# Performance work log

Hardware: AMD Instinct MI355X
Metric: run time of the kernel (lower is better)

The kernel has to match this reference:

```python
import jax, jax.numpy as jnp
import numpy as np

D_TEXT, D_AUDIO, D_HID = 1024, 768, 1024
EPS = 1e-5


def layer_norm(x, gamma, beta):
    mu = jnp.mean(x, axis=-1, keepdims=True)
    var = jnp.mean(jnp.square(x - mu), axis=-1, keepdims=True)
    return (x - mu) * jax.lax.rsqrt(var + EPS) * gamma + beta


def setup_inputs() -> dict:
    key = jax.random.key(0)
    ks = jax.random.split(key, 8)
    B, L, S = 16, 1024, 2048
    # xavier_uniform bound = sqrt(6/(fan_in+fan_out))
    def xavier(k, shape):
        bound = np.sqrt(6.0 / (shape[0] + shape[1]))
        return jax.random.uniform(k, shape, jnp.float32, -bound, bound)
    return {
        "H_l": jax.random.normal(ks[0], (B, L, D_TEXT), jnp.float32),
        "H_a": jax.random.normal(ks[1], (B, S, D_AUDIO), jnp.float32),
        "W_text": xavier(ks[2], (D_TEXT, D_HID)),
        "b_text": jnp.zeros((D_HID,), jnp.float32),
        "W_audio": xavier(ks[3], (D_AUDIO, D_HID)),
        "b_audio": jnp.zeros((D_HID,), jnp.float32),
        "W_out": xavier(ks[4], (D_HID, D_HID)),
        "b_out": jnp.zeros((D_HID,), jnp.float32),
        "g1": jnp.ones((D_HID,), jnp.float32),
        "beta1": jnp.zeros((D_HID,), jnp.float32),
        "g2": jnp.ones((D_HID,), jnp.float32),
        "beta2": jnp.zeros((D_HID,), jnp.float32),
        "g_out": jnp.ones((D_HID,), jnp.float32),
        "beta_out": jnp.zeros((D_HID,), jnp.float32),
    }


def reference(H_l, H_a, W_text, b_text, W_audio, b_audio, W_out, b_out,
              g1, beta1, g2, beta2, g_out, beta_out):
    # projections
    text_p = jnp.einsum('bld,dh->blh', H_l, W_text) + b_text    # [B,L,H]
    audio_p = jnp.einsum('bsd,dh->bsh', H_a, W_audio) + b_audio  # [B,S,H]
    Q = layer_norm(text_p, g1, beta1)
    K = layer_norm(audio_p, g2, beta2)
    V = audio_p
    scale = 1.0 / np.sqrt(D_HID).astype(np.float32)
    scores = jnp.einsum('blh,bsh->bls', Q, K) * scale            # [B,L,S]
    alpha = jax.nn.softmax(scores, axis=-1)
    # dropout is identity in eval mode
    H_hyper = jnp.einsum('bls,bsh->blh', alpha, V)               # [B,L,H]
    H_hyper = jnp.einsum('blh,hk->blk', H_hyper, W_out) + b_out
    return layer_norm(H_hyper + H_l, g_out, beta_out)
```

## Files before the change

### kernel.cpp

```cpp
#include <hip/hip_runtime.h>
#include <cstdio>

typedef unsigned short u16;
typedef __bf16 bf16x8 __attribute__((ext_vector_type(8)));
typedef float f32x4 __attribute__((ext_vector_type(4)));
typedef unsigned short us4 __attribute__((ext_vector_type(4)));
typedef unsigned short us8 __attribute__((ext_vector_type(8)));

__device__ __forceinline__ u16 f2bf(float f) {
    union { float f; unsigned u; } x; x.f = f;
    unsigned u = x.u + 0x7fffu + ((x.u >> 16) & 1u);
    return (u16)(u >> 16);
}
__device__ __forceinline__ float bf2f(u16 u) {
    union { unsigned u; float f; } x; x.u = ((unsigned)u) << 16;
    return x.f;
}


#define LDFRAG(base, row, koff) \
  (*(const bf16x8*)((const char*)(base) + (size_t)(row) * 128 + \
                    ((koff) ^ (((row) & 7) << 4))))

#define BAR() do { \
  asm volatile("" ::: "memory"); \
  __builtin_amdgcn_s_barrier(); \
  asm volatile("" ::: "memory"); \
} while (0)

#define LGKM0() asm volatile("s_waitcnt lgkmcnt(0)" ::: "memory")

#define MFMA16(AF, BF, MO, NO) do { \
  __builtin_amdgcn_s_setprio(1); \
  _Pragma("unroll") for (int j = 0; j < 4; ++j) \
    _Pragma("unroll") for (int i = 0; i < 2; ++i) \
      _Pragma("unroll") for (int ks = 0; ks < 2; ++ks) \
        acc[(MO) + j][(NO) + i] = __builtin_amdgcn_mfma_f32_16x16x32_bf16( \
            AF[j][ks], BF[i][ks], acc[(MO) + j][(NO) + i], 0, 0, 0); \
  __builtin_amdgcn_s_setprio(0); \
} while (0)

template<int TAG, bool HAS_BIAS, bool HAS_RESID, bool OUT_BF16, bool EMIT_VT>
__global__ __launch_bounds__(512, 2)
void gemm_nt(const u16* __restrict__ A, const u16* __restrict__ Bm,
             void* __restrict__ Cm, const float* __restrict__ bias,
             const float* __restrict__ resid, u16* __restrict__ vt,
             int K, int lda, int ldb, int ldc,
             long sA, long sB, long sC, float scale)
{
    __shared__ __align__(16) u16 lA[4 * 128 * 64];
    __shared__ __align__(16) u16 lB[4 * 128 * 64];

    const int tid = threadIdx.x;

    const int gx = gridDim.x, gy = gridDim.y;
    int flat = ((int)blockIdx.z * gy + blockIdx.y) * gx + blockIdx.x;
    const int nwg = gx * gy * (int)gridDim.z;
    const int q = nwg >> 3;
    flat = (flat & 7) * q + (flat >> 3);
    const int bx = flat % gx;
    const int t2 = flat / gx;
    const int by = t2 % gy;
    const long bz = t2 / gy;

    A  += bz * sA;
    Bm += bz * sB;
    const long cbase = bz * sC;
    const int m0 = by * 256;
    const int n0 = bx * 256;

    const int lane = tid & 63;
    const int w  = tid >> 6;
    const int wr = w >> 2, wc = w & 3;
    const int fr = lane & 15;
    const int kg = lane >> 4;

    auto stage_half = [&](int kt, int op, int h) {
        const u16* src = op ? Bm : A;
        const int  ld  = op ? ldb : lda;
        const int  bs  = op ? n0 : m0;
        u16* lds = (op ? lB : lA) + (size_t)(((2 * kt + h) & 3)) * 8192;
#pragma unroll
        for (int i2 = 0; i2 < 2; ++i2) {
            const int c  = i2 * 512 + tid;
            const int r  = c >> 3;
            const int kb = ((c & 7) * 16) ^ ((r & 7) << 4);
            const u16* g = src + (size_t)(bs + h * 128 + r) * ld + kt * 64 + (kb >> 1);
            __builtin_amdgcn_global_load_lds(
                (const __attribute__((address_space(1))) void*)g,
                (__attribute__((address_space(3))) void*)(lds + (size_t)c * 8), 16, 0, 0);
        }
    };
    auto stage_tile = [&](int kt) {
        stage_half(kt, 0, 0); stage_half(kt, 0, 1);
        stage_half(kt, 1, 0); stage_half(kt, 1, 1);
    };

    f32x4 acc[8][4] = {};

    const int nt = K >> 6;
    stage_tile(0);
    stage_tile(1);

    const int bRowBase = (wc & 1) * 64;

    for (int T = 0; T < nt; ++T) {
        if (T == nt - 1) asm volatile("s_waitcnt vmcnt(0)" ::: "memory");
        else             asm volatile("s_waitcnt vmcnt(8)" ::: "memory");
        BAR();

        const u16* pA = lA + (size_t)(((2 * T + wr) & 3)) * 8192;
        const u16* pB = lB + (size_t)(((2 * T + (wc >> 1)) & 3)) * 8192;
        const bool pre = (T + 2 < nt);

        bf16x8 af0[4][2], af1[4][2], bfr0[2][2], bfr1[2][2];

#pragma unroll
        for (int j = 0; j < 4; ++j)
#pragma unroll
            for (int ks = 0; ks < 2; ++ks)
                af0[j][ks] = LDFRAG(pA, j * 16 + fr, ks * 64 + kg * 16);
#pragma unroll
        for (int i = 0; i < 2; ++i)
#pragma unroll
            for (int ks = 0; ks < 2; ++ks)
                bfr0[i][ks] = LDFRAG(pB, bRowBase + i * 16 + fr, ks * 64 + kg * 16);
        BAR();
        LGKM0();
        MFMA16(af0, bfr0, 0, 0);
        BAR();

#pragma unroll
        for (int i = 0; i < 2; ++i)
#pragma unroll
            for (int ks = 0; ks < 2; ++ks)
                bfr1[i][ks] = LDFRAG(pB, bRowBase + 32 + i * 16 + fr, ks * 64 + kg * 16);
        BAR();
        LGKM0();
        MFMA16(af0, bfr1, 0, 2);
        BAR();

#pragma unroll
        for (int j = 0; j < 4; ++j)
#pragma unroll
            for (int ks = 0; ks < 2; ++ks)
                af1[j][ks] = LDFRAG(pA, 64 + j * 16 + fr, ks * 64 + kg * 16);
        if (pre) { stage_half(T + 2, 1, 0); stage_half(T + 2, 1, 1); }
        BAR();
        LGKM0();
        MFMA16(af1, bfr0, 4, 0);
        BAR();

        if (pre) { stage_half(T + 2, 0, 0); stage_half(T + 2, 0, 1); }
        MFMA16(af1, bfr1, 4, 2);
    }

    const int orow = m0 + wr * 128 + kg * 4;
    const int ocol = n0 + wc * 64 + fr;
#pragma unroll
    for (int mf = 0; mf < 8; ++mf) {
        const int mbase = orow + mf * 16;
#pragma unroll
        for (int nf = 0; nf < 4; ++nf) {
            const int n = ocol + nf * 16;
            float v4[4];
#pragma unroll
            for (int r = 0; r < 4; ++r) {
                const int m = mbase + r;
                float v = acc[mf][nf][r] * scale;
                if (HAS_BIAS)  v += bias[n];
                if (HAS_RESID) v += resid[cbase + (long)m * ldc + n];
                v4[r] = v;
                if (OUT_BF16)  ((u16*)Cm)[cbase + (long)m * ldc + n] = f2bf(v);
                else           ((float*)Cm)[cbase + (long)m * ldc + n] = v;
            }
            if (EMIT_VT) {
                const long b_ = mbase >> 11;
                const int  s  = mbase & 2047;
                us4 o;
#pragma unroll
                for (int r = 0; r < 4; ++r) o[r] = f2bf(v4[r]);
                *(us4*)(vt + (b_ * 1024 + n) * 2048 + s) = o;
            }
        }
    }
}

template<bool IN_BF16, bool OUT_BF16>
__global__ __launch_bounds__(256)
void ln1024(const void* in, const float* __restrict__ g,
            const float* __restrict__ beta, void* out)
{
    const long row = blockIdx.x;
    const int tid = threadIdx.x;
    float x0, x1, x2, x3;
    if (IN_BF16) {
        const us4 v = ((const us4*)in)[row * 256 + tid];
        x0 = bf2f(v[0]); x1 = bf2f(v[1]); x2 = bf2f(v[2]); x3 = bf2f(v[3]);
    } else {
        const float4 v = ((const float4*)in)[row * 256 + tid];
        x0 = v.x; x1 = v.y; x2 = v.z; x3 = v.w;
    }
    float s  = x0 + x1 + x2 + x3;
    float s2 = x0 * x0 + x1 * x1 + x2 * x2 + x3 * x3;
#pragma unroll
    for (int off = 32; off > 0; off >>= 1) {
        s  += __shfl_xor(s, off);
        s2 += __shfl_xor(s2, off);
    }
    __shared__ float rs[4], rq[4];
    if ((tid & 63) == 0) { rs[tid >> 6] = s; rq[tid >> 6] = s2; }
    __syncthreads();
    const float S  = rs[0] + rs[1] + rs[2] + rs[3];
    const float S2 = rq[0] + rq[1] + rq[2] + rq[3];
    const float mu = S * (1.0f / 1024.0f);
    const float var = S2 * (1.0f / 1024.0f) - mu * mu;
    const float rstd = rsqrtf(var + 1e-5f);
    const float4 gg = ((const float4*)g)[tid];
    const float4 bb = ((const float4*)beta)[tid];
    const float y0 = (x0 - mu) * rstd * gg.x + bb.x;
    const float y1 = (x1 - mu) * rstd * gg.y + bb.y;
    const float y2 = (x2 - mu) * rstd * gg.z + bb.z;
    const float y3 = (x3 - mu) * rstd * gg.w + bb.w;
    if (OUT_BF16) {
        us4 o; o[0] = f2bf(y0); o[1] = f2bf(y1); o[2] = f2bf(y2); o[3] = f2bf(y3);
        ((us4*)out)[row * 256 + tid] = o;
    } else {
        float4 o; o.x = y0; o.y = y1; o.z = y2; o.w = y3;
        ((float4*)out)[row * 256 + tid] = o;
    }
}

__global__ __launch_bounds__(256)
void softmax2048_bf16(u16* io)
{
    const long row = blockIdx.x;
    const int tid = threadIdx.x;
    const us8 v = ((const us8*)io)[row * 256 + tid];
    float x[8];
#pragma unroll
    for (int i = 0; i < 8; ++i) x[i] = bf2f(v[i]);
    float m = x[0];
#pragma unroll
    for (int i = 1; i < 8; ++i) m = fmaxf(m, x[i]);
#pragma unroll
    for (int off = 32; off > 0; off >>= 1) m = fmaxf(m, __shfl_xor(m, off));
    __shared__ float rm[4], rsum[4];
    if ((tid & 63) == 0) rm[tid >> 6] = m;
    __syncthreads();
    m = fmaxf(fmaxf(rm[0], rm[1]), fmaxf(rm[2], rm[3]));
    float e[8];
    float s = 0.f;
#pragma unroll
    for (int i = 0; i < 8; ++i) { e[i] = __expf(x[i] - m); s += e[i]; }
#pragma unroll
    for (int off = 32; off > 0; off >>= 1) s += __shfl_xor(s, off);
    if ((tid & 63) == 0) rsum[tid >> 6] = s;
    __syncthreads();
    s = rsum[0] + rsum[1] + rsum[2] + rsum[3];
    const float inv = 1.0f / s;
    us8 o;
#pragma unroll
    for (int i = 0; i < 8; ++i) o[i] = f2bf(e[i] * inv);
    ((us8*)io)[row * 256 + tid] = o;
}

__global__ __launch_bounds__(256)
void cast2_f32_bf16(const float* __restrict__ srcA, u16* __restrict__ dstA, long nA8,
                    const float* __restrict__ srcB, u16* __restrict__ dstB, long nB8)
{
    long i = (long)blockIdx.x * 256 + threadIdx.x;
    const float* in;
    u16* out;
    if (i < nA8) { in = srcA; out = dstA; }
    else         { i -= nA8; if (i >= nB8) return; in = srcB; out = dstB; }
    const float4 a = ((const float4*)in)[i * 2];
    const float4 b = ((const float4*)in)[i * 2 + 1];
    us8 o;
    o[0] = f2bf(a.x); o[1] = f2bf(a.y); o[2] = f2bf(a.z); o[3] = f2bf(a.w);
    o[4] = f2bf(b.x); o[5] = f2bf(b.y); o[6] = f2bf(b.z); o[7] = f2bf(b.w);
    ((us8*)out)[i] = o;
}

__global__ __launch_bounds__(256)
void tcast3_f32_bf16(const float* __restrict__ w0, u16* __restrict__ t0,
                     const float* __restrict__ w1, u16* __restrict__ t1,
                     const float* __restrict__ w2, u16* __restrict__ t2)
{
    const int z = blockIdx.z;
    const float* in; u16* out; int R;
    if      (z == 0) { in = w0; out = t0; R = 1024; }
    else if (z == 1) { in = w1; out = t1; R = 768;  }
    else             { in = w2; out = t2; R = 1024; }
    const int C = 1024;
    const int r0 = blockIdx.y * 32;
    if (r0 >= R) return;
    __shared__ float t[32][33];
    const int tx = threadIdx.x, ty = threadIdx.y;
    const int c0 = blockIdx.x * 32;
#pragma unroll
    for (int i = 0; i < 4; ++i)
        t[ty + i * 8][tx] = in[(long)(r0 + ty + i * 8) * C + c0 + tx];
    __syncthreads();
#pragma unroll
    for (int i = 0; i < 4; ++i)
        out[(long)(c0 + ty + i * 8) * R + r0 + tx] = f2bf(t[tx][ty + i * 8]);
}

extern "C" void kernel_launch(void* const* d_in, const int* in_sizes, int n_in,
                              void* d_out, int out_size, void* d_ws, size_t ws_size,
                              hipStream_t stream)
{
    const float* H_l      = (const float*)d_in[0];
    const float* H_a      = (const float*)d_in[1];
    const float* W_text   = (const float*)d_in[2];
    const float* b_text   = (const float*)d_in[3];
    const float* W_audio  = (const float*)d_in[4];
    const float* b_audio  = (const float*)d_in[5];
    const float* W_out    = (const float*)d_in[6];
    const float* b_out    = (const float*)d_in[7];
    const float* g1       = (const float*)d_in[8];
    const float* beta1    = (const float*)d_in[9];
    const float* g2       = (const float*)d_in[10];
    const float* beta2    = (const float*)d_in[11];
    const float* g_out    = (const float*)d_in[12];
    const float* beta_out = (const float*)d_in[13];
    (void)in_sizes; (void)n_in; (void)out_size;

    const int B = 16, L = 1024, S = 2048, DT = 1024, DA = 768, H = 1024;

    char* ws = (char*)d_ws;
    const size_t SZ_HLB = (size_t)B * L * DT * 2;
    const size_t SZ_HAB = (size_t)B * S * DA * 2;
    const size_t O_A    = SZ_HLB + SZ_HAB;
    const size_t SZ_A   = (size_t)B * L * H * 2;
    const size_t O_C    = O_A + SZ_A;
    const size_t SZ_C   = (size_t)B * S * H * 2;
    const size_t O_D    = O_C + SZ_C;
    const size_t SZ_D   = (size_t)B * S * H * 2;
    const size_t O_W    = O_D + SZ_D;
    const size_t need   = O_W + (size_t)(DT * H + DA * H + H * H) * 2;

    if (ws_size < need) {
        fprintf(stderr, "[kernel_launch] ws_size=%zu < needed=%zu — aborting launches\n",
                ws_size, need);
        return;
    }

    u16*   Hlb     = (u16*)(ws);
    u16*   Hab     = (u16*)(ws + SZ_HLB);
    u16*   Scores  = (u16*)(ws);
    u16*   Abuf    = (u16*)(ws + O_A);
    u16*   Vbuf    = (u16*)(ws + O_C);
    u16*   Kbuf    = (u16*)(ws + O_D);
    u16*   OutPre  = (u16*)(ws + O_D);
    u16*   Wt_text  = (u16*)(ws + O_W);
    u16*   Wt_audio = Wt_text + (size_t)DT * H;
    u16*   Wt_out   = Wt_audio + (size_t)DA * H;
    u16*   Vt      = (u16*)d_out;

    const float scale = 0.03125f;

    const long nHl8 = (long)B * L * DT / 8;
    const long nHa8 = (long)B * S * DA / 8;
    cast2_f32_bf16<<<(unsigned)((nHl8 + nHa8 + 255) / 256), 256, 0, stream>>>(
        H_l, Hlb, nHl8, H_a, Hab, nHa8);
    tcast3_f32_bf16<<<dim3(H / 32, 32, 3), dim3(32, 8), 0, stream>>>(
        W_text, Wt_text, W_audio, Wt_audio, W_out, Wt_out);

    gemm_nt<1, true, false, true, false><<<dim3(H / 256, B * L / 256, 1), 512, 0, stream>>>(
        Hlb, Wt_text, Abuf, b_text, nullptr, nullptr, DT, DT, DT, H, 0, 0, 0, 1.0f);
    ln1024<true, true><<<B * L, 256, 0, stream>>>(Abuf, g1, beta1, Abuf);

    gemm_nt<2, true, false, true, true><<<dim3(H / 256, B * S / 256, 1), 512, 0, stream>>>(
        Hab, Wt_audio, Vbuf, b_audio, nullptr, Vt, DA, DA, DA, H, 0, 0, 0, 1.0f);
    ln1024<true, true><<<B * S, 256, 0, stream>>>(Vbuf, g2, beta2, Kbuf);

    gemm_nt<3, false, false, true, false><<<dim3(S / 256, L / 256, B), 512, 0, stream>>>(
        Abuf, Kbuf, Scores, nullptr, nullptr, nullptr, H, H, H, S,
        (long)L * H, (long)S * H, (long)L * S, scale);

    softmax2048_bf16<<<B * L, 256, 0, stream>>>(Scores);

    gemm_nt<5, false, false, true, false><<<dim3(H / 256, L / 256, B), 512, 0, stream>>>(
        Scores, Vt, Abuf, nullptr, nullptr, nullptr, S, S, S, H,
        (long)L * S, (long)H * S, (long)L * H, 1.0f);

    gemm_nt<6, true, true, true, false><<<dim3(H / 256, B * L / 256, 1), 512, 0, stream>>>(
        Abuf, Wt_out, OutPre, b_out, H_l, nullptr, H, H, H, H, 0, 0, 0, 1.0f);

    ln1024<true, false><<<B * L, 256, 0, stream>>>(OutPre, g_out, beta_out, (float*)d_out);
}
```

Baseline: 473.3 us.

## Restructure GEMM LDS pipeline to half-tile granular double buffering

The GEMM main loop changes from prefetching whole k-tiles two steps ahead, with one vmcnt wait per tile, to staging the next tile in quarter pieces interleaved across the four MFMA phases. Each phase now ends with a finer vmcnt wait, so the data needed by the next phase is ready just in time. This spreads global-to-LDS traffic evenly over the compute and lets the first tile start earlier. In exchange the prefetch distance drops from two tiles to one, so latency hiding becomes tighter and each iteration gains extra barriers.

```diff
diff --git a/kernel.cpp b/kernel.cpp
--- a/kernel.cpp
+++ b/kernel.cpp
@@ -29,6 +29,9 @@
 } while (0)
 
 #define LGKM0() asm volatile("s_waitcnt lgkmcnt(0)" ::: "memory")
+#define VMC4()  asm volatile("s_waitcnt vmcnt(4)" ::: "memory")
+#define VMC2()  asm volatile("s_waitcnt vmcnt(2)" ::: "memory")
+#define VMC0()  asm volatile("s_waitcnt vmcnt(0)" ::: "memory")
 
 #define MFMA16(AF, BF, MO, NO) do { \
   __builtin_amdgcn_s_setprio(1); \
@@ -79,7 +82,7 @@
         const u16* src = op ? Bm : A;
         const int  ld  = op ? ldb : lda;
         const int  bs  = op ? n0 : m0;
-        u16* lds = (op ? lB : lA) + (size_t)(((2 * kt + h) & 3)) * 8192;
+        u16* lds = (op ? lB : lA) + (size_t)((kt & 1) * 2 + h) * 8192;
 #pragma unroll
         for (int i2 = 0; i2 < 2; ++i2) {
             const int c  = i2 * 512 + tid;
@@ -91,27 +94,22 @@
                 (__attribute__((address_space(3))) void*)(lds + (size_t)c * 8), 16, 0, 0);
         }
     };
-    auto stage_tile = [&](int kt) {
-        stage_half(kt, 0, 0); stage_half(kt, 0, 1);
-        stage_half(kt, 1, 0); stage_half(kt, 1, 1);
-    };
 
     f32x4 acc[8][4] = {};
 
     const int nt = K >> 6;
-    stage_tile(0);
-    stage_tile(1);
+    stage_half(0, 0, 0); stage_half(0, 1, 0);
+    stage_half(0, 1, 1); stage_half(0, 0, 1);
+    VMC4();
+    BAR();
 
     const int bRowBase = (wc & 1) * 64;
 
     for (int T = 0; T < nt; ++T) {
-        if (T == nt - 1) asm volatile("s_waitcnt vmcnt(0)" ::: "memory");
-        else             asm volatile("s_waitcnt vmcnt(8)" ::: "memory");
-        BAR();
-
-        const u16* pA = lA + (size_t)(((2 * T + wr) & 3)) * 8192;
-        const u16* pB = lB + (size_t)(((2 * T + (wc >> 1)) & 3)) * 8192;
-        const bool pre = (T + 2 < nt);
+        const int d = T & 1;
+        const u16* pA = lA + (size_t)(d * 2 + wr) * 8192;
+        const u16* pB = lB + (size_t)(d * 2 + (wc >> 1)) * 8192;
+        const bool pre = (T + 1 < nt);
 
         bf16x8 af0[4][2], af1[4][2], bfr0[2][2], bfr1[2][2];
 
@@ -125,9 +123,11 @@
 #pragma unroll
             for (int ks = 0; ks < 2; ++ks)
                 bfr0[i][ks] = LDFRAG(pB, bRowBase + i * 16 + fr, ks * 64 + kg * 16);
+        if (pre) stage_half(T + 1, 0, 0);
         BAR();
         LGKM0();
         MFMA16(af0, bfr0, 0, 0);
+        if (pre) VMC4(); else VMC2();
         BAR();
 
 #pragma unroll
@@ -135,9 +135,11 @@
 #pragma unroll
             for (int ks = 0; ks < 2; ++ks)
                 bfr1[i][ks] = LDFRAG(pB, bRowBase + 32 + i * 16 + fr, ks * 64 + kg * 16);
+        if (pre) stage_half(T + 1, 1, 0);
         BAR();
         LGKM0();
         MFMA16(af0, bfr1, 0, 2);
+        if (pre) VMC4(); else VMC0();
         BAR();
 
 #pragma unroll
@@ -145,14 +147,16 @@
 #pragma unroll
             for (int ks = 0; ks < 2; ++ks)
                 af1[j][ks] = LDFRAG(pA, 64 + j * 16 + fr, ks * 64 + kg * 16);
-        if (pre) { stage_half(T + 2, 1, 0); stage_half(T + 2, 1, 1); }
+        if (pre) stage_half(T + 1, 1, 1);
         BAR();
         LGKM0();
         MFMA16(af1, bfr0, 4, 0);
         BAR();
 
-        if (pre) { stage_half(T + 2, 0, 0); stage_half(T + 2, 0, 1); }
+        if (pre) stage_half(T + 1, 0, 1);
         MFMA16(af1, bfr1, 4, 2);
+        if (pre) VMC4();
+        BAR();
     }
 
     const int orow = m0 + wr * 128 + kg * 4;
```

After: 474.1 us (median of 2 runs). Within noise of the previous version (+0.2%).
